# Optimization experiments

Measured on AMD Instinct MI355X. Metric: run time of the kernel, lower is better.

## Reference

```python
import jax, jax.numpy as jnp
import numpy as np

NHEADS = 16
KVHEADS = 4
HEAD_DIM = 128  # emb_kq_per_head == emb_v_per_head
ROPE_THETA = 10000.0


def _rotary(x, cos, sin):
    # x: [B, S, H, D]; half-split rotation
    x1, x2 = jnp.split(x, 2, axis=-1)
    rot = jnp.concatenate([-x2, x1], axis=-1)
    return x * cos + rot * sin


def setup_inputs() -> dict:
    key = jax.random.key(0)
    k1, k2, k3 = jax.random.split(key, 3)
    B, S, E = 2, 2048, 2048
    qkv_out = NHEADS * HEAD_DIM + 2 * KVHEADS * HEAD_DIM  # 3072
    return {
        "x": jax.random.normal(k1, (B, S, E), dtype=jnp.float32),
        "w_qkv": jax.random.normal(k2, (E, qkv_out), dtype=jnp.float32) * 0.02,
        "w_dense": jax.random.normal(k3, (NHEADS * HEAD_DIM, E), dtype=jnp.float32) * 0.02,
    }


def reference(x, w_qkv, w_dense):
    B, S, E = x.shape
    D = HEAD_DIM
    # fused QKV projection (use_bias=False), then split per FusedQKV.splits
    qkv = x @ w_qkv  # [B, S, 3072]
    q, k, v = jnp.split(qkv, [NHEADS * D, NHEADS * D + KVHEADS * D], axis=-1)
    q = q.reshape(B, S, NHEADS, D)
    k = k.reshape(B, S, KVHEADS, D)
    v = v.reshape(B, S, KVHEADS, D)

    # rotary position encoding, positions = arange(S)
    pos = jnp.arange(S, dtype=jnp.float32)
    inv_freq = 1.0 / (ROPE_THETA ** (jnp.arange(0, D, 2, dtype=jnp.float32) / D))
    ang = pos[:, None] * inv_freq[None, :]                 # [S, D/2]
    ang = jnp.concatenate([ang, ang], axis=-1)             # [S, D]
    cos = jnp.cos(ang)[None, :, None, :]                   # [1, S, 1, D]
    sin = jnp.sin(ang)[None, :, None, :]
    q = _rotary(q, cos, sin)
    k = _rotary(k, cos, sin)

    # GQA: expand kv heads to query heads
    rep = NHEADS // KVHEADS
    k = jnp.repeat(k, rep, axis=2)  # [B, S, NHEADS, D]
    v = jnp.repeat(v, rep, axis=2)

    scale = 1.0 / jnp.sqrt(jnp.asarray(D, dtype=x.dtype))
    scores = jnp.einsum("bqhd,bkhd->bhqk", q, k) * scale   # [B, H, S, S]
    causal = jnp.tril(jnp.ones((S, S), dtype=bool))
    scores = jnp.where(causal[None, None], scores, jnp.finfo(scores.dtype).min)
    probs = jax.nn.softmax(scores, axis=-1)
    attn = jnp.einsum("bhqk,bkhd->bqhd", probs, v)         # [B, S, H, D]
    attn = attn.reshape(B, S, NHEADS * D)
    return attn @ w_dense                                  # [B, S, E]
```

## Files before the change

kernel.cpp:

```cpp
#include <hip/hip_runtime.h>
#include <type_traits>


typedef __attribute__((ext_vector_type(8))) short short8;
typedef __attribute__((ext_vector_type(4))) float floatx4;
typedef __attribute__((ext_vector_type(4))) unsigned short ushort4v;
typedef __attribute__((ext_vector_type(4))) unsigned int uint4v;

constexpr int NH    = 16;
constexpr int NKV   = 4;
constexpr int HD    = 128;
constexpr int SEQ   = 2048;
constexpr int EMB   = 2048;
constexpr int NBATCH = 2;
constexpr int MROWS = NBATCH * SEQ;
constexpr int NQKV  = (NH + 2 * NKV) * HD;

__device__ __forceinline__ unsigned short f2b(float f) {
  union { float f; unsigned u; } v; v.f = f;
  unsigned u = v.u + 0x7FFFu + ((v.u >> 16) & 1u);
  return (unsigned short)(u >> 16);
}
__device__ __forceinline__ float b2f(unsigned short h) {
  union { unsigned u; float f; } v; v.u = (unsigned)h << 16;
  return v.f;
}

__device__ __forceinline__ void gload_lds16(const unsigned short* g,
                                            unsigned short* lds) {
  __builtin_amdgcn_global_load_lds(
      (const __attribute__((address_space(1))) unsigned int*)g,
      (__attribute__((address_space(3))) unsigned int*)lds, 16, 0, 0);
}

__global__ void cvt_f32_bf16(const float* __restrict__ in,
                             unsigned short* __restrict__ out, int n) {
  int i = (blockIdx.x * 256 + threadIdx.x) * 4;
  if (i + 3 < n) {
    floatx4 v = *(const floatx4*)(in + i);
    ushort4v o = { f2b(v[0]), f2b(v[1]), f2b(v[2]), f2b(v[3]) };
    *(ushort4v*)(out + i) = o;
  }
}

__global__ void transpose_cvt_dual(const float* __restrict__ wqkv,
                                   unsigned short* __restrict__ oqkv,
                                   const float* __restrict__ wd,
                                   unsigned short* __restrict__ od) {
  const int z = blockIdx.z;
  const float* in = z ? wd : wqkv;
  unsigned short* out = z ? od : oqkv;
  const int R = EMB;
  const int C = z ? EMB : NQKV;
  int c0 = blockIdx.x * 32, r0 = blockIdx.y * 32;
  if (c0 >= C) return;
  __shared__ float t[32][33];
  int tx = threadIdx.x & 31, ty = threadIdx.x >> 5;
#pragma unroll
  for (int i = 0; i < 32; i += 8)
    t[ty + i][tx] = in[(long)(r0 + ty + i) * C + (c0 + tx)];
  __syncthreads();
#pragma unroll
  for (int i = 0; i < 32; i += 8)
    out[(long)(c0 + ty + i) * R + (r0 + tx)] = f2b(t[tx][ty + i]);
}

constexpr int BM = 128, BK = 64;

template <int MODE>
__global__ __launch_bounds__(256, MODE == 1 ? 4 : 3) void gemm_bt(
    const unsigned short* __restrict__ A,
    const unsigned short* __restrict__ BT,
    int Mdim, int Ndim, int Kdim,
    float* __restrict__ outF,
    unsigned short* __restrict__ Qb,
    unsigned short* __restrict__ Kb,
    unsigned short* __restrict__ Vt,
    float qscale) {
  constexpr int TBN = (MODE == 1) ? 64 : 128;
  constexpr int NI  = TBN / 32;
  __shared__ __align__(16) unsigned short smem[BM * BK + TBN * BK];
  unsigned short (*As)[BK] = (unsigned short (*)[BK])smem;
  unsigned short (*Bs)[BK] = (unsigned short (*)[BK])(smem + BM * BK);
  const int tid = threadIdx.x;
  const int bm = blockIdx.y * BM;
  const int bn = blockIdx.x * TBN;
  const int wave = tid >> 6, lane = tid & 63;
  const int l = lane & 15, q = lane >> 4;
  const int l7 = l & 7;
  const int wm = (wave >> 1) * 64, wn = (wave & 1) * (TBN / 2);

  floatx4 acc[4][NI] = {};

  const int srow = lane >> 3;
  const int scol = ((lane & 7) ^ srow) * 8;
  const unsigned short* Arow = A + (long)bm * Kdim;
  const unsigned short* Brow = BT + (long)bn * Kdim;

  for (int k0 = 0; k0 < Kdim; k0 += BK) {
#pragma unroll
    for (int i = 0; i < 4; ++i) {
      const int r0 = wave * 32 + i * 8;
      gload_lds16(Arow + (long)(r0 + srow) * Kdim + k0 + scol, &As[r0][0]);
    }
#pragma unroll
    for (int i = 0; i < TBN / 32; ++i) {
      const int r0 = wave * (TBN / 4) + i * 8;
      gload_lds16(Brow + (long)(r0 + srow) * Kdim + k0 + scol, &Bs[r0][0]);
    }
    __syncthreads();
#pragma unroll
    for (int kk = 0; kk < 2; ++kk) {
      short8 af[4], bfr[NI];
#pragma unroll
      for (int mi = 0; mi < 4; ++mi)
        af[mi] = *(const short8*)&As[wm + mi * 16 + l][((kk * 4 + q) ^ l7) * 8];
#pragma unroll
      for (int ni = 0; ni < NI; ++ni)
        bfr[ni] = *(const short8*)&Bs[wn + ni * 16 + l][((kk * 4 + q) ^ l7) * 8];
#pragma unroll
      for (int mi = 0; mi < 4; ++mi)
#pragma unroll
        for (int ni = 0; ni < NI; ++ni)
          acc[mi][ni] = __builtin_amdgcn_mfma_f32_16x16x32_bf16(
              af[mi], bfr[ni], acc[mi][ni], 0, 0, 0);
    }
    __syncthreads();
  }

  if constexpr (MODE == 1) {
#pragma unroll
    for (int mi = 0; mi < 4; ++mi) {
      const int rowbase = bm + wm + mi * 16 + q * 4;
#pragma unroll
      for (int ni = 0; ni < NI; ++ni) {
        const int col = bn + wn + ni * 16 + l;
#pragma unroll
        for (int r = 0; r < 4; ++r)
          outF[(long)(rowbase + r) * Ndim + col] = acc[mi][ni][r];
      }
    }
  } else if (bn >= (NH + NKV) * HD) {
    const int hh = (bn - (NH + NKV) * HD) >> 7;
#pragma unroll
    for (int mi = 0; mi < 4; ++mi) {
      const int m0 = bm + wm + mi * 16 + q * 4;
      const int bb = m0 >> 11, s = m0 & (SEQ - 1);
      const int s6 = s & 63;
      const int p6 = (s6 & 32) | ((s6 & 12) << 1) | ((s6 & 16) >> 2);
      const int sp = (s & ~63) | p6;
      unsigned short* vtb = Vt + ((long)(bb * NKV + hh)) * HD * SEQ;
#pragma unroll
      for (int ni = 0; ni < NI; ++ni) {
        const int d = wn + ni * 16 + l;
        ushort4v pv = { f2b(acc[mi][ni][0]), f2b(acc[mi][ni][1]),
                        f2b(acc[mi][ni][2]), f2b(acc[mi][ni][3]) };
        *(ushort4v*)(vtb + (long)d * SEQ + sp) = pv;
      }
    }
  } else {
    unsigned short (*Ct)[128] = (unsigned short (*)[128])smem;
#pragma unroll
    for (int mi = 0; mi < 4; ++mi)
#pragma unroll
      for (int ni = 0; ni < NI; ++ni)
#pragma unroll
        for (int r = 0; r < 4; ++r) {
          const int row = wm + mi * 16 + q * 4 + r;
          const int col = wn + ni * 16 + l;
          const int cs = ((((col >> 3) ^ row) & 7) | (col & 64 ? 8 : 0)) * 8 + (col & 7);
          Ct[row][cs] = f2b(acc[mi][ni][r]);
        }
    __syncthreads();
    const int row = tid >> 1, g = tid & 1;
    const int m = bm + row, bb = m >> 11, s = m & (SEQ - 1);
    const bool isQ = (bn < NH * HD);
    unsigned short* dst;
    if (isQ) dst = Qb + (((long)(bb * NH + (bn >> 7))) * SEQ + s) * HD;
    else     dst = Kb + (((long)(bb * NKV + ((bn - NH * HD) >> 7))) * SEQ + s) * HD;
    const float scale = isQ ? qscale : 1.0f;
    const float sf = (float)s;
#pragma unroll
    for (int i = 0; i < 8; ++i) {
      const int lbo = g * 8 + i;
      const int lbx = (g ^ 1) * 8 + i;
      const int pbo = (lbo & 8) | ((lbo ^ row) & 7);
      const int pbx = (lbx & 8) | ((lbx ^ row) & 7);
      short8 xo = *(const short8*)&Ct[row][pbo * 8];
      short8 xx = *(const short8*)&Ct[row][pbx * 8];
      short8 outv;
#pragma unroll
      for (int j2 = 0; j2 < 8; ++j2) {
        const int j = i * 8 + j2;
        const float e = -(float)j * (2.0f * 13.287712379549449f / 128.0f);
        const float ang = sf * exp2f(e);
        float sn, cs_;
        sincosf(ang, &sn, &cs_);
        const float xown = b2f((unsigned short)xo[j2]);
        const float xoth = b2f((unsigned short)xx[j2]);
        const float rr = g ? (xown * cs_ + xoth * sn)
                           : (xown * cs_ - xoth * sn);
        outv[j2] = (short)f2b(rr * scale);
      }
      *(short8*)(dst + g * 64 + i * 8) = outv;
    }
  }
}

__global__ __launch_bounds__(256, 2) void attn_kernel(
    const unsigned short* __restrict__ Q,
    const unsigned short* __restrict__ K,
    const unsigned short* __restrict__ VT,
    unsigned short* __restrict__ attn) {
  const int h = blockIdx.y, b = blockIdx.z;
  const int t = b ? (15 - (int)blockIdx.x) : (int)blockIdx.x;
  const int kvh = h >> 2;
  const int tid = threadIdx.x;
  const int wave = tid >> 6, lane = tid & 63;
  const int l = lane & 15, q = lane >> 4;
  const int l7 = l & 7;
  const int wq = wave * 32;

  const unsigned short* Kh  = K  + ((long)(b * NKV + kvh)) * SEQ * HD;
  const unsigned short* VTh = VT + ((long)(b * NKV + kvh)) * HD * SEQ;

  __shared__ __align__(16) unsigned short smem[2 * 64 * 128 + 2 * 128 * 64];
  unsigned short (*Ks)[64 * 128]  = (unsigned short (*)[64 * 128])smem;
  unsigned short (*VTs)[128 * 64] = (unsigned short (*)[128 * 64])(smem + 2 * 64 * 128);

  int koff[4], voff[4];
  {
    const int k_rl = lane >> 4, k_bp = lane & 15;
    const int v_rl = lane >> 3, v_bp = lane & 7;
#pragma unroll
    for (int j = 0; j < 4; ++j) {
      const int rk = (wave * 4 + j) * 4 + k_rl;
      koff[j] = rk * HD + (k_bp ^ (rk & 15)) * 8;
      const int rv = (wave * 4 + j) * 8 + v_rl;
      voff[j] = rv * SEQ + (v_bp ^ (rv & 7)) * 8;
    }
  }

  short8 onesf;
#pragma unroll
  for (int i = 0; i < 8; ++i) onesf[i] = (short)0x3F80;

  auto stage = [&](int c, int buf) {
    const unsigned short* kc = Kh + c * (64 * HD);
    const unsigned short* vc = VTh + c * 64;
#pragma unroll
    for (int j = 0; j < 4; ++j)
      gload_lds16(kc + koff[j], &Ks[buf][(wave * 4 + j) * 4 * 128]);
#pragma unroll
    for (int j = 0; j < 4; ++j)
      gload_lds16(vc + voff[j], &VTs[buf][(wave * 4 + j) * 8 * 64]);
  };

  const unsigned short* Qh = Q + (((long)(b * NH + h)) * SEQ + t * 128) * HD;
  short8 qf[2][4];
#pragma unroll
  for (int mh = 0; mh < 2; ++mh)
#pragma unroll
    for (int kk = 0; kk < 4; ++kk)
      qf[mh][kk] = *(const short8*)(Qh + (long)(wq + mh * 16 + l) * HD + kk * 32 + q * 8);

  floatx4 o[2][9] = {};

  auto chunk_body = [&](auto masked, int cur, int kv0) {
    constexpr bool MASKED = decltype(masked)::value;
    floatx4 sf[2][4] = {};
#pragma unroll
    for (int kk = 0; kk < 4; ++kk) {
      short8 kf[4];
#pragma unroll
      for (int ni = 0; ni < 4; ++ni)
        kf[ni] = *(const short8*)&Ks[cur][(ni * 16 + l) * 128 + (((kk * 4 + q) ^ l) * 8)];
#pragma unroll
      for (int mh = 0; mh < 2; ++mh)
#pragma unroll
        for (int ni = 0; ni < 4; ++ni)
          sf[mh][ni] = __builtin_amdgcn_mfma_f32_16x16x32_bf16(
              kf[ni], qf[mh][kk], sf[mh][ni], 0, 0, 0);
    }
    short8 pf[2][2];
#pragma unroll
    for (int mh = 0; mh < 2; ++mh) {
      const int qrow = t * 128 + wq + mh * 16 + l;
      unsigned u[8];
#pragma unroll
      for (int ni = 0; ni < 4; ++ni) {
        if constexpr (MASKED) {
#pragma unroll
          for (int r = 0; r < 4; ++r)
            if (kv0 + ni * 16 + q * 4 + r > qrow) sf[mh][ni][r] = -3e38f;
        }
        float e0 = exp2f(sf[mh][ni][0]);
        float e1 = exp2f(sf[mh][ni][1]);
        float e2 = exp2f(sf[mh][ni][2]);
        float e3 = exp2f(sf[mh][ni][3]);
        asm("v_cvt_pk_bf16_f32 %0, %1, %2" : "=v"(u[ni * 2]) : "v"(e0), "v"(e1));
        asm("v_cvt_pk_bf16_f32 %0, %1, %2" : "=v"(u[ni * 2 + 1]) : "v"(e2), "v"(e3));
      }
      union { uint4v v; short8 s; } a0, a1;
      a0.v = (uint4v){u[0], u[1], u[2], u[3]};
      a1.v = (uint4v){u[4], u[5], u[6], u[7]};
      pf[mh][0] = a0.s;
      pf[mh][1] = a1.s;
    }
#pragma unroll
    for (int c2 = 0; c2 < 2; ++c2) {
      const int pb = ((c2 * 4 + q) ^ l7) * 8;
#pragma unroll
      for (int di = 0; di < 8; ++di) {
        short8 vf = *(const short8*)&VTs[cur][(di * 16 + l) * 64 + pb];
        o[0][di] = __builtin_amdgcn_mfma_f32_16x16x32_bf16(pf[0][c2], vf, o[0][di], 0, 0, 0);
        o[1][di] = __builtin_amdgcn_mfma_f32_16x16x32_bf16(pf[1][c2], vf, o[1][di], 0, 0, 0);
      }
      o[0][8] = __builtin_amdgcn_mfma_f32_16x16x32_bf16(pf[0][c2], onesf, o[0][8], 0, 0, 0);
      o[1][8] = __builtin_amdgcn_mfma_f32_16x16x32_bf16(pf[1][c2], onesf, o[1][8], 0, 0, 0);
    }
  };

  const int nc = 2 * t + 2;
  stage(0, 0);
  __syncthreads();

  int c = 0;
#pragma unroll 1
  for (; c < nc - 2; ++c) {
    stage(c + 1, (c & 1) ^ 1);
    chunk_body(std::false_type{}, c & 1, c * 64);
    __syncthreads();
  }
  stage(c + 1, (c & 1) ^ 1);
  chunk_body(std::true_type{}, c & 1, c * 64);
  __syncthreads();
  ++c;
  chunk_body(std::true_type{}, c & 1, c * 64);
  __syncthreads();

  unsigned short (*Ob)[136] = (unsigned short (*)[136])smem;
#pragma unroll
  for (int mh = 0; mh < 2; ++mh)
#pragma unroll
    for (int r = 0; r < 4; ++r) {
      const float inv = 1.0f / o[mh][8][r];
#pragma unroll
      for (int di = 0; di < 8; ++di)
        Ob[wq + mh * 16 + q * 4 + r][di * 16 + l] = f2b(o[mh][di][r] * inv);
    }
  __syncthreads();
  {
    const int row = tid >> 1, g = (tid & 1) * 64;
    const int s = t * 128 + row;
    unsigned short* dst = attn + ((long)(b * SEQ + s)) * (NH * HD) + h * HD + g;
#pragma unroll
    for (int j = 0; j < 8; ++j)
      *(short8*)(dst + j * 8) = *(const short8*)&Ob[row][g + j * 8];
  }
}

extern "C" void kernel_launch(void* const* d_in, const int* in_sizes, int n_in,
                              void* d_out, int out_size, void* d_ws, size_t ws_size,
                              hipStream_t stream) {
  const float* x       = (const float*)d_in[0];
  const float* w_qkv   = (const float*)d_in[1];
  const float* w_dense = (const float*)d_in[2];
  float* out = (float*)d_out;

  char* ws = (char*)d_ws;
  const size_t MB = 1024 * 1024;
  unsigned short* xb    = (unsigned short*)(ws);
  unsigned short* wqkvT = (unsigned short*)(ws + 16 * MB);
  unsigned short* wdT   = (unsigned short*)(ws + 28 * MB);
  unsigned short* Qb    = (unsigned short*)(ws + 36 * MB);
  unsigned short* Kb    = (unsigned short*)(ws + 52 * MB);
  unsigned short* VTb   = (unsigned short*)(ws + 56 * MB);
  unsigned short* attn  = xb;

  const float qscale = 0.08838834764831845f * 1.4426950408889634f;

  cvt_f32_bf16<<<(MROWS * EMB) / (256 * 4), 256, 0, stream>>>(x, xb, MROWS * EMB);
  transpose_cvt_dual<<<dim3(NQKV / 32, EMB / 32, 2), 256, 0, stream>>>(
      w_qkv, wqkvT, w_dense, wdT);

  gemm_bt<0><<<dim3(NQKV / 128, MROWS / BM), 256, 0, stream>>>(
      xb, wqkvT, MROWS, NQKV, EMB, nullptr, Qb, Kb, VTb, qscale);

  attn_kernel<<<dim3(16, NH, NBATCH), 256, 0, stream>>>(Qb, Kb, VTb, attn);

  gemm_bt<1><<<dim3(EMB / 64, MROWS / BM), 256, 0, stream>>>(
      attn, wdT, MROWS, EMB, NH * HD, out, nullptr, nullptr, nullptr, 0.0f);
}
```

Before: 282.1 us.

## Precompute RoPE cos/sin table and stage V-transpose epilogue through LDS

```diff
diff --git a/kernel.cpp b/kernel.cpp
--- a/kernel.cpp
+++ b/kernel.cpp
@@ -41,6 +41,17 @@
     ushort4v o = { f2b(v[0]), f2b(v[1]), f2b(v[2]), f2b(v[3]) };
     *(ushort4v*)(out + i) = o;
   }
+}
+
+__global__ void rope_table(float* __restrict__ tab) {
+  int idx = blockIdx.x * 256 + threadIdx.x;
+  int j = idx & 63, s = idx >> 6;
+  float e = -(float)j * (2.0f * 13.287712379549449f / 128.0f);
+  float ang = (float)s * exp2f(e);
+  float sn, c;
+  sincosf(ang, &sn, &c);
+  tab[idx * 2]     = c;
+  tab[idx * 2 + 1] = sn;
 }
 
 __global__ void transpose_cvt_dual(const float* __restrict__ wqkv,
@@ -76,6 +87,7 @@
     unsigned short* __restrict__ Qb,
     unsigned short* __restrict__ Kb,
     unsigned short* __restrict__ Vt,
+    const float* __restrict__ ropetab,
     float qscale) {
   constexpr int TBN = (MODE == 1) ? 64 : 128;
   constexpr int NI  = TBN / 32;
@@ -140,38 +152,45 @@
           outF[(long)(rowbase + r) * Ndim + col] = acc[mi][ni][r];
       }
     }
-  } else if (bn >= (NH + NKV) * HD) {
+    return;
+  }
+
+  unsigned short (*Ct)[128] = (unsigned short (*)[128])smem;
+#pragma unroll
+  for (int mi = 0; mi < 4; ++mi)
+#pragma unroll
+    for (int ni = 0; ni < NI; ++ni)
+#pragma unroll
+      for (int r = 0; r < 4; ++r) {
+        const int row = wm + mi * 16 + q * 4 + r;
+        const int col = wn + ni * 16 + l;
+        const int cs = ((((col >> 3) ^ row) & 7) | (col & 64 ? 8 : 0)) * 8 + (col & 7);
+        Ct[row][cs] = f2b(acc[mi][ni][r]);
+      }
+  __syncthreads();
+
+  if (bn >= (NH + NKV) * HD) {
     const int hh = (bn - (NH + NKV) * HD) >> 7;
-#pragma unroll
-    for (int mi = 0; mi < 4; ++mi) {
-      const int m0 = bm + wm + mi * 16 + q * 4;
-      const int bb = m0 >> 11, s = m0 & (SEQ - 1);
-      const int s6 = s & 63;
-      const int p6 = (s6 & 32) | ((s6 & 12) << 1) | ((s6 & 16) >> 2);
-      const int sp = (s & ~63) | p6;
-      unsigned short* vtb = Vt + ((long)(bb * NKV + hh)) * HD * SEQ;
-#pragma unroll
-      for (int ni = 0; ni < NI; ++ni) {
-        const int d = wn + ni * 16 + l;
-        ushort4v pv = { f2b(acc[mi][ni][0]), f2b(acc[mi][ni][1]),
-                        f2b(acc[mi][ni][2]), f2b(acc[mi][ni][3]) };
-        *(ushort4v*)(vtb + (long)d * SEQ + sp) = pv;
-      }
+    const int d = tid >> 1, ch = tid & 1;
+    const int m0 = bm + ch * 64;
+    const int bb = m0 >> 11, sbase = m0 & (SEQ - 1);
+    unsigned short* vrow =
+        Vt + ((long)(bb * NKV + hh)) * HD * SEQ + (long)d * SEQ + sbase;
+    const int dblk = d >> 3, dlo = d & 7, dhi = (d & 64) ? 8 : 0;
+#pragma unroll
+    for (int pb = 0; pb < 8; ++pb) {
+      short8 ov;
+#pragma unroll
+      for (int j = 0; j < 8; ++j) {
+        const int p6 = pb * 8 + j;
+        const int s6 = (p6 & 32) | ((p6 & 24) >> 1) | ((p6 & 4) << 2) | (p6 & 3);
+        const int row = ch * 64 + s6;
+        const int cs = (((dblk ^ row) & 7) | dhi) * 8 + dlo;
+        ov[j] = (short)Ct[row][cs];
+      }
+      *(short8*)(vrow + pb * 8) = ov;
     }
   } else {
-    unsigned short (*Ct)[128] = (unsigned short (*)[128])smem;
-#pragma unroll
-    for (int mi = 0; mi < 4; ++mi)
-#pragma unroll
-      for (int ni = 0; ni < NI; ++ni)
-#pragma unroll
-        for (int r = 0; r < 4; ++r) {
-          const int row = wm + mi * 16 + q * 4 + r;
-          const int col = wn + ni * 16 + l;
-          const int cs = ((((col >> 3) ^ row) & 7) | (col & 64 ? 8 : 0)) * 8 + (col & 7);
-          Ct[row][cs] = f2b(acc[mi][ni][r]);
-        }
-    __syncthreads();
     const int row = tid >> 1, g = tid & 1;
     const int m = bm + row, bb = m >> 11, s = m & (SEQ - 1);
     const bool isQ = (bn < NH * HD);
@@ -179,7 +198,7 @@
     if (isQ) dst = Qb + (((long)(bb * NH + (bn >> 7))) * SEQ + s) * HD;
     else     dst = Kb + (((long)(bb * NKV + ((bn - NH * HD) >> 7))) * SEQ + s) * HD;
     const float scale = isQ ? qscale : 1.0f;
-    const float sf = (float)s;
+    const float* trow = ropetab + (long)s * 128;
 #pragma unroll
     for (int i = 0; i < 8; ++i) {
       const int lbo = g * 8 + i;
@@ -188,18 +207,19 @@
       const int pbx = (lbx & 8) | ((lbx ^ row) & 7);
       short8 xo = *(const short8*)&Ct[row][pbo * 8];
       short8 xx = *(const short8*)&Ct[row][pbx * 8];
+      floatx4 t0 = *(const floatx4*)(trow + i * 16);
+      floatx4 t1 = *(const floatx4*)(trow + i * 16 + 4);
+      floatx4 t2 = *(const floatx4*)(trow + i * 16 + 8);
+      floatx4 t3 = *(const floatx4*)(trow + i * 16 + 12);
+      const float cc[8] = { t0[0], t0[2], t1[0], t1[2], t2[0], t2[2], t3[0], t3[2] };
+      const float ss[8] = { t0[1], t0[3], t1[1], t1[3], t2[1], t2[3], t3[1], t3[3] };
       short8 outv;
 #pragma unroll
       for (int j2 = 0; j2 < 8; ++j2) {
-        const int j = i * 8 + j2;
-        const float e = -(float)j * (2.0f * 13.287712379549449f / 128.0f);
-        const float ang = sf * exp2f(e);
-        float sn, cs_;
-        sincosf(ang, &sn, &cs_);
         const float xown = b2f((unsigned short)xo[j2]);
         const float xoth = b2f((unsigned short)xx[j2]);
-        const float rr = g ? (xown * cs_ + xoth * sn)
-                           : (xown * cs_ - xoth * sn);
+        const float rr = g ? (xown * cc[j2] + xoth * ss[j2])
+                           : (xown * cc[j2] - xoth * ss[j2]);
         outv[j2] = (short)f2b(rr * scale);
       }
       *(short8*)(dst + g * 64 + i * 8) = outv;
@@ -376,19 +396,21 @@
   unsigned short* Qb    = (unsigned short*)(ws + 36 * MB);
   unsigned short* Kb    = (unsigned short*)(ws + 52 * MB);
   unsigned short* VTb   = (unsigned short*)(ws + 56 * MB);
+  float*          rtab  = (float*)(ws + 60 * MB);
   unsigned short* attn  = xb;
 
   const float qscale = 0.08838834764831845f * 1.4426950408889634f;
 
+  rope_table<<<(SEQ * 64) / 256, 256, 0, stream>>>(rtab);
   cvt_f32_bf16<<<(MROWS * EMB) / (256 * 4), 256, 0, stream>>>(x, xb, MROWS * EMB);
   transpose_cvt_dual<<<dim3(NQKV / 32, EMB / 32, 2), 256, 0, stream>>>(
       w_qkv, wqkvT, w_dense, wdT);
 
   gemm_bt<0><<<dim3(NQKV / 128, MROWS / BM), 256, 0, stream>>>(
-      xb, wqkvT, MROWS, NQKV, EMB, nullptr, Qb, Kb, VTb, qscale);
+      xb, wqkvT, MROWS, NQKV, EMB, nullptr, Qb, Kb, VTb, rtab, qscale);
 
   attn_kernel<<<dim3(16, NH, NBATCH), 256, 0, stream>>>(Qb, Kb, VTb, attn);
 
   gemm_bt<1><<<dim3(EMB / 64, MROWS / BM), 256, 0, stream>>>(
-      attn, wdT, MROWS, EMB, NH * HD, out, nullptr, nullptr, nullptr, 0.0f);
-}
+      attn, wdT, MROWS, EMB, NH * HD, out, nullptr, nullptr, nullptr, nullptr, 0.0f);
+}
```

New measurement: 275.3 us. 1.02x faster.
